# Kernel optimization log

Hardware: AMD Instinct MI355X
Metric: run time of the kernel (lower is better)

## Reference

```python
import jax, jax.numpy as jnp
import numpy as np

B, IN_CH, SLOTS, SLOT_SIZE, READ_SLOTS = 16, 512, 10000, 256, 3


def _fa_params(key, c, scale=0.02):
    k1, k2 = jax.random.split(key)
    return (jax.random.normal(k1, (c, c), jnp.float32) * scale, jnp.zeros((c,), jnp.float32),
            jax.random.normal(k2, (c, c), jnp.float32) * scale, jnp.zeros((c,), jnp.float32))


def fast_attention(x, w1, b1, w2, b2):
    # FastAttention: x * Linear2(softmax(Linear1(x), dim=channel))
    h = jax.nn.softmax(x @ w1 + b1, axis=1)
    return x * (h @ w2 + b2)


def setup_inputs() -> dict:
    key = jax.random.key(0)
    ks = jax.random.split(key, 12)
    s = 0.02
    inp = {}
    inp["inputs"] = jax.random.normal(ks[0], (B, IN_CH), jnp.float32)
    inp["memory"] = jax.random.normal(ks[1], (B, SLOTS, SLOT_SIZE), jnp.float32)
    # read_weights branch: FastAttention(IN_CH) -> Linear(IN_CH, READ_SLOTS*SLOTS) -> tanh
    inp["fa_r_w1"], inp["fa_r_b1"], inp["fa_r_w2"], inp["fa_r_b2"] = _fa_params(ks[2], IN_CH)
    inp["W_read"] = jax.random.normal(ks[3], (IN_CH, READ_SLOTS * SLOTS), jnp.float32) * s
    inp["b_read"] = jnp.zeros((READ_SLOTS * SLOTS,), jnp.float32)
    # update_weights branch: FastAttention(IN_CH) -> Linear(IN_CH, READ_SLOTS) -> sigmoid
    inp["fa_u_w1"], inp["fa_u_b1"], inp["fa_u_w2"], inp["fa_u_b2"] = _fa_params(ks[4], IN_CH)
    inp["W_uw"] = jax.random.normal(ks[5], (IN_CH, READ_SLOTS), jnp.float32) * s
    inp["b_uw"] = jnp.zeros((READ_SLOTS,), jnp.float32)
    # update_memory branch: FastAttention(IN_CH+SLOT_SIZE) -> Linear(., SLOT_SIZE) -> relu
    inp["fa_um_w1"], inp["fa_um_b1"], inp["fa_um_w2"], inp["fa_um_b2"] = _fa_params(ks[6], IN_CH + SLOT_SIZE)
    inp["W_um"] = jax.random.normal(ks[7], (IN_CH + SLOT_SIZE, SLOT_SIZE), jnp.float32) * s
    inp["b_um"] = jnp.zeros((SLOT_SIZE,), jnp.float32)
    # apply_memory branch: FastAttention(2*SLOT_SIZE) -> Linear(., SLOT_SIZE) -> relu
    inp["fa_am_w1"], inp["fa_am_b1"], inp["fa_am_w2"], inp["fa_am_b2"] = _fa_params(ks[8], 2 * SLOT_SIZE)
    inp["W_am"] = jax.random.normal(ks[9], (2 * SLOT_SIZE, SLOT_SIZE), jnp.float32) * s
    inp["b_am"] = jnp.zeros((SLOT_SIZE,), jnp.float32)
    return inp


def reference(inputs, memory,
              fa_r_w1, fa_r_b1, fa_r_w2, fa_r_b2, W_read, b_read,
              fa_u_w1, fa_u_b1, fa_u_w2, fa_u_b2, W_uw, b_uw,
              fa_um_w1, fa_um_b1, fa_um_w2, fa_um_b2, W_um, b_um,
              fa_am_w1, fa_am_b1, fa_am_w2, fa_am_b2, W_am, b_am):
    b = inputs.shape[0]
    # read scores: [B, READ_SLOTS, SLOTS]
    read = jnp.tanh(fast_attention(inputs, fa_r_w1, fa_r_b1, fa_r_w2, fa_r_b2) @ W_read + b_read)
    read = read.reshape(b, READ_SLOTS, SLOTS)
    read_w = jnp.max(read, axis=2)                 # [B, READ_SLOTS]
    read_idx = jnp.argmax(read, axis=2)            # [B, READ_SLOTS] int
    upd_w = jax.nn.sigmoid(fast_attention(inputs, fa_u_w1, fa_u_b1, fa_u_w2, fa_u_b2) @ W_uw + b_uw)
    # gather the selected memory slots: [B, READ_SLOTS, SLOT_SIZE]
    r_all = memory[jnp.arange(b)[:, None], read_idx]
    m = jnp.zeros((b, SLOT_SIZE), inputs.dtype)
    # sequential recurrence over the (small, fixed) read_slots
    for i in range(READ_SLOTS):
        r = r_all[:, i]                            # [B, SLOT_SIZE]
        upd = jax.nn.relu(fast_attention(jnp.concatenate([r, inputs], axis=1),
                                         fa_um_w1, fa_um_b1, fa_um_w2, fa_um_b2) @ W_um + b_um)
        u = upd_w[:, i:i + 1]
        r = u * upd + (1.0 - u) * r
        m = read_w[:, i:i + 1] * jax.nn.relu(fast_attention(jnp.concatenate([r, m], axis=1),
                                                            fa_am_w1, fa_am_b1, fa_am_w2, fa_am_b2) @ W_am + b_am)
    return jnp.tanh(m)
```

## Files before the change

kernel.cpp:

```cpp
#include <hip/hip_runtime.h>
#include <cfloat>
#include <cmath>

constexpr int NTILES = 79;

enum : int {
  WS_XR    = 0,
  WS_UPDW  = 8192,
  WS_READW = 8240,
  WS_PMAX  = 8288,
  WS_PIDX  = 12080,
  WS_RNEW  = 15872,
  WS_M     = 28160,
  WS_XC    = 32256,
  WS_TPA   = 69120,
  WS_HA    = 134656,
  WS_YPA   = 151040,
  WS_TPU   = 216576,
  WS_HU    = 437760,
  WS_YPU   = 474624,
  WS_WPU   = 695808,
  WS_TPM   = 769536,
  WS_HM    = 802304,
  WS_YPM   = 810496,
  WS_WPM   = 843264,
};

__device__ __forceinline__ float wave_sum(float v) {
#pragma unroll
  for (int o = 32; o > 0; o >>= 1) v += __shfl_xor(v, o);
  return v;
}
__device__ __forceinline__ float wave_max(float v) {
#pragma unroll
  for (int o = 32; o > 0; o >>= 1) v = fmaxf(v, __shfl_xor(v, o));
  return v;
}
__device__ __forceinline__ float block_sum(float v, float* red) {
  int lane = threadIdx.x & 63, w = threadIdx.x >> 6, nw = blockDim.x >> 6;
  v = wave_sum(v);
  __syncthreads();
  if (lane == 0) red[w] = v;
  __syncthreads();
  float s = 0.f;
  for (int k = 0; k < nw; k++) s += red[k];
  return s;
}
__device__ __forceinline__ float block_max(float v, float* red) {
  int lane = threadIdx.x & 63, w = threadIdx.x >> 6, nw = blockDim.x >> 6;
  v = wave_max(v);
  __syncthreads();
  if (lane == 0) red[w] = v;
  __syncthreads();
  float s = -FLT_MAX;
  for (int k = 0; k < nw; k++) s = fmaxf(s, red[k]);
  return s;
}

__device__ __forceinline__ void mm_tile16(
    const float* __restrict__ xs,
    const float* __restrict__ W, int ldw,
    int koff, int jbase, float2& ra, float2& rb) {
  int lane = threadIdx.x & 63, w = threadIdx.x >> 6;
  const float* xa = xs + (w * 2) * 128;
  const float* xb = xa + 128;
  const float* Wp = W + (size_t)koff * ldw + jbase + lane * 2;
  float a00 = 0.f, a01 = 0.f, a10 = 0.f, a11 = 0.f;
#pragma unroll 8
  for (int k = 0; k < 128; k++) {
    float2 wv = *(const float2*)(Wp + (size_t)k * ldw);
    float xav = xa[k], xbv = xb[k];
    a00 = fmaf(xav, wv.x, a00); a01 = fmaf(xav, wv.y, a01);
    a10 = fmaf(xbv, wv.x, a10); a11 = fmaf(xbv, wv.y, a11);
  }
  ra = make_float2(a00, a01);
  rb = make_float2(a10, a11);
}
__device__ __forceinline__ void store_tile16(
    float* __restrict__ T, int ldt, int jbase, float2 ra, float2 rb) {
  int lane = threadIdx.x & 63, w = threadIdx.x >> 6;
  int r0 = w * 2, j0 = jbase + lane * 2;
  *(float2*)(T + (size_t)r0 * ldt + j0) = ra;
  *(float2*)(T + (size_t)(r0 + 1) * ldt + j0) = rb;
}

__global__ __launch_bounds__(512) void k_mm1_a(
    const float* __restrict__ x, const float* __restrict__ w1r,
    const float* __restrict__ w1u, float* __restrict__ TPA) {
  __shared__ float xs[16 * 128];
  int jt = blockIdx.x, ks = blockIdx.y, m = blockIdx.z, tid = threadIdx.x;
  for (int t = tid; t < 2048; t += 512) {
    int b = t >> 7, kk = t & 127;
    xs[t] = x[b * 512 + ks * 128 + kk];
  }
  __syncthreads();
  float2 ra, rb;
  mm_tile16(xs, m ? w1u : w1r, 512, ks * 128, jt * 128, ra, rb);
  store_tile16(TPA + (size_t)((m * 4 + ks) * 16) * 512, 512, jt * 128, ra, rb);
}

__global__ __launch_bounds__(512) void k_sm_a(
    const float* __restrict__ TPA, const float* __restrict__ b1r,
    const float* __restrict__ b1u, float* __restrict__ HA) {
  __shared__ float red[16];
  int b = blockIdx.x, m = blockIdx.y, tid = threadIdx.x;
  float t = (m ? b1u : b1r)[tid];
#pragma unroll
  for (int ks = 0; ks < 4; ks++)
    t += TPA[(size_t)((m * 4 + ks) * 16 + b) * 512 + tid];
  float mx = block_max(t, red);
  float e = expf(t - mx);
  float s = block_sum(e, red);
  HA[(size_t)(m * 16 + b) * 512 + tid] = e / s;
}

__global__ __launch_bounds__(512) void k_mm2_a(
    const float* __restrict__ HA, const float* __restrict__ w2r,
    const float* __restrict__ w2u, float* __restrict__ YPA) {
  __shared__ float xs[16 * 128];
  int jt = blockIdx.x, ks = blockIdx.y, m = blockIdx.z, tid = threadIdx.x;
  for (int t = tid; t < 2048; t += 512) {
    int b = t >> 7, kk = t & 127;
    xs[t] = HA[(size_t)(m * 16 + b) * 512 + ks * 128 + kk];
  }
  __syncthreads();
  float2 ra, rb;
  mm_tile16(xs, m ? w2u : w2r, 512, ks * 128, jt * 128, ra, rb);
  store_tile16(YPA + (size_t)((m * 4 + ks) * 16) * 512, 512, jt * 128, ra, rb);
}

__global__ __launch_bounds__(512) void k_fin_a(
    const float* __restrict__ x, const float* __restrict__ YPA,
    const float* __restrict__ b2r, const float* __restrict__ b2u,
    const float* __restrict__ Wuw, const float* __restrict__ buw,
    float* __restrict__ XR, float* __restrict__ UPDW, float* __restrict__ M) {
  __shared__ float red[16];
  int b = blockIdx.x, tid = threadIdx.x;
  float yr = b2r[tid], yu = b2u[tid];
#pragma unroll
  for (int ks = 0; ks < 4; ks++) {
    yr += YPA[(size_t)((0 + ks) * 16 + b) * 512 + tid];
    yu += YPA[(size_t)((4 + ks) * 16 + b) * 512 + tid];
  }
  float xv = x[b * 512 + tid];
  XR[b * 512 + tid] = xv * yr;
  float xu = xv * yu;
  if (tid < 256) M[b * 256 + tid] = 0.f;
  for (int i = 0; i < 3; i++) {
    float si = block_sum(xu * Wuw[tid * 3 + i], red);
    if (tid == 0) UPDW[b * 3 + i] = 1.f / (1.f + expf(-(si + buw[i])));
  }
}

__global__ __launch_bounds__(512) void k_read(
    const float* __restrict__ W, const float* __restrict__ brd,
    const float* __restrict__ xr,
    float* __restrict__ pmax, int* __restrict__ pidx) {
  __shared__ __align__(16) float xs[16 * 512];
  int tid = threadIdx.x, lane = tid & 63, w = tid >> 6;
  int i = blockIdx.y, tile = blockIdx.x;
  {
    const float4* s4 = (const float4*)xr;
    float4* d4 = (float4*)xs;
    for (int t = tid; t < 2048; t += 512) d4[t] = s4[t];
  }
  __syncthreads();
  int b0 = w * 2, b1 = b0 + 1;
  int s0 = tile * 128 + lane * 2;
  int sC = (s0 > 9998) ? 9998 : s0;
  const float* Wp = W + i * 10000 + sC;
  const float* xap = xs + b0 * 512;
  const float* xbp = xs + b1 * 512;
  float a00 = 0.f, a01 = 0.f, a10 = 0.f, a11 = 0.f;
#pragma unroll 8
  for (int c = 0; c < 512; c += 4) {
    float4 xa = *(const float4*)(xap + c);
    float4 xb = *(const float4*)(xbp + c);
    float2 w0 = *(const float2*)(Wp + (size_t)(c + 0) * 30000);
    float2 w1 = *(const float2*)(Wp + (size_t)(c + 1) * 30000);
    float2 w2 = *(const float2*)(Wp + (size_t)(c + 2) * 30000);
    float2 w3 = *(const float2*)(Wp + (size_t)(c + 3) * 30000);
    a00 = fmaf(xa.x, w0.x, a00); a01 = fmaf(xa.x, w0.y, a01);
    a10 = fmaf(xb.x, w0.x, a10); a11 = fmaf(xb.x, w0.y, a11);
    a00 = fmaf(xa.y, w1.x, a00); a01 = fmaf(xa.y, w1.y, a01);
    a10 = fmaf(xb.y, w1.x, a10); a11 = fmaf(xb.y, w1.y, a11);
    a00 = fmaf(xa.z, w2.x, a00); a01 = fmaf(xa.z, w2.y, a01);
    a10 = fmaf(xb.z, w2.x, a10); a11 = fmaf(xb.z, w2.y, a11);
    a00 = fmaf(xa.w, w3.x, a00); a01 = fmaf(xa.w, w3.y, a01);
    a10 = fmaf(xb.w, w3.x, a10); a11 = fmaf(xb.w, w3.y, a11);
  }
  float2 bb = *(const float2*)(brd + i * 10000 + sC);
  bool ok0 = (s0 < 10000), ok1 = (s0 + 1 < 10000);
  float v00 = a00 + bb.x, v01 = a01 + bb.y;
  float v10 = a10 + bb.x, v11 = a11 + bb.y;
  float bv0 = ok0 ? v00 : -FLT_MAX; int bi0 = s0;
  if (ok1 && v01 > bv0) { bv0 = v01; bi0 = s0 + 1; }
  float bv1 = ok0 ? v10 : -FLT_MAX; int bi1 = s0;
  if (ok1 && v11 > bv1) { bv1 = v11; bi1 = s0 + 1; }
#pragma unroll
  for (int o = 32; o > 0; o >>= 1) {
    float ov = __shfl_down(bv0, o); int oi = __shfl_down(bi0, o);
    if (ov > bv0) { bv0 = ov; bi0 = oi; }
    ov = __shfl_down(bv1, o); oi = __shfl_down(bi1, o);
    if (ov > bv1) { bv1 = ov; bi1 = oi; }
  }
  if (lane == 0) {
    int base = (i * 16 + b0) * NTILES + tile;
    pmax[base] = bv0; pidx[base] = bi0;
    base = (i * 16 + b1) * NTILES + tile;
    pmax[base] = bv1; pidx[base] = bi1;
  }
}

__global__ __launch_bounds__(768) void k_gather(
    const float* __restrict__ mem, const float* __restrict__ x,
    const float* __restrict__ pmax, const int* __restrict__ pidx,
    float* __restrict__ READW, float* __restrict__ XC) {
  __shared__ int sidx;
  int bi = blockIdx.x, b = bi / 3, i = bi % 3;
  int tid = threadIdx.x, lane = tid & 63;
  if (tid < 64) {
    float bv = -FLT_MAX; int bix = 0;
    const float* pm = pmax + (i * 16 + b) * NTILES;
    const int* pi = pidx + (i * 16 + b) * NTILES;
    for (int t = lane; t < NTILES; t += 64) {
      float v = pm[t]; int ix = pi[t];
      if (v > bv || (v == bv && ix < bix)) { bv = v; bix = ix; }
    }
#pragma unroll
    for (int o = 32; o > 0; o >>= 1) {
      float ov = __shfl_down(bv, o); int oi = __shfl_down(bix, o);
      if (ov > bv || (ov == bv && oi < bix)) { bv = ov; bix = oi; }
    }
    if (lane == 0) { sidx = bix; READW[bi] = tanhf(bv); }
  }
  __syncthreads();
  if (tid < 256) XC[(size_t)bi * 768 + tid] = mem[((size_t)b * 10000 + sidx) * 256 + tid];
  else           XC[(size_t)bi * 768 + tid] = x[b * 512 + (tid - 256)];
}

__global__ __launch_bounds__(512) void k_mm1_u(
    const float* __restrict__ XC, const float* __restrict__ w1um,
    float* __restrict__ TPU) {
  __shared__ float xs[16 * 128];
  int jt = blockIdx.x, ks = blockIdx.y, g = blockIdx.z, tid = threadIdx.x;
  for (int t = tid; t < 2048; t += 512) {
    int r = t >> 7, kk = t & 127;
    xs[t] = XC[(size_t)(g * 16 + r) * 768 + ks * 128 + kk];
  }
  __syncthreads();
  float2 ra, rb;
  mm_tile16(xs, w1um, 768, ks * 128, jt * 128, ra, rb);
  store_tile16(TPU + (size_t)(ks * 48 + g * 16) * 768, 768, jt * 128, ra, rb);
}

__global__ __launch_bounds__(768) void k_sm_u(
    const float* __restrict__ TPU, const float* __restrict__ b1um,
    float* __restrict__ HU) {
  __shared__ float red[16];
  int bi = blockIdx.x, tid = threadIdx.x;
  float t = b1um[tid];
#pragma unroll
  for (int ks = 0; ks < 6; ks++)
    t += TPU[(size_t)(ks * 48 + bi) * 768 + tid];
  float mx = block_max(t, red);
  float e = expf(t - mx);
  float s = block_sum(e, red);
  HU[(size_t)bi * 768 + tid] = e / s;
}

__global__ __launch_bounds__(512) void k_mm2_u(
    const float* __restrict__ HU, const float* __restrict__ w2um,
    float* __restrict__ YPU) {
  __shared__ float xs[16 * 128];
  int jt = blockIdx.x, ks = blockIdx.y, g = blockIdx.z, tid = threadIdx.x;
  for (int t = tid; t < 2048; t += 512) {
    int r = t >> 7, kk = t & 127;
    xs[t] = HU[(size_t)(g * 16 + r) * 768 + ks * 128 + kk];
  }
  __syncthreads();
  float2 ra, rb;
  mm_tile16(xs, w2um, 768, ks * 128, jt * 128, ra, rb);
  store_tile16(YPU + (size_t)(ks * 48 + g * 16) * 768, 768, jt * 128, ra, rb);
}

__global__ __launch_bounds__(512) void k_wum(
    const float* __restrict__ YPU, const float* __restrict__ XC,
    const float* __restrict__ b2um, const float* __restrict__ Wum,
    float* __restrict__ WPU) {
  __shared__ float xs[16 * 128];
  int jt = blockIdx.x, ks = blockIdx.y, g = blockIdx.z, tid = threadIdx.x;
  for (int t = tid; t < 2048; t += 512) {
    int r = t >> 7, kk = t & 127;
    int bi = g * 16 + r, k = ks * 128 + kk;
    float y = b2um[k];
#pragma unroll
    for (int k2 = 0; k2 < 6; k2++) y += YPU[(size_t)(k2 * 48 + bi) * 768 + k];
    xs[t] = XC[(size_t)bi * 768 + k] * y;
  }
  __syncthreads();
  float2 ra, rb;
  mm_tile16(xs, Wum, 256, ks * 128, jt * 128, ra, rb);
  store_tile16(WPU + (size_t)(ks * 48 + g * 16) * 256, 256, jt * 128, ra, rb);
}

__global__ __launch_bounds__(256) void k_fin_u(
    const float* __restrict__ WPU, const float* __restrict__ XC,
    const float* __restrict__ bum, const float* __restrict__ UPDW,
    float* __restrict__ RNEW) {
  int bi = blockIdx.x, tid = threadIdx.x;
  float s = bum[tid];
#pragma unroll
  for (int ks = 0; ks < 6; ks++)
    s += WPU[(size_t)(ks * 48 + bi) * 256 + tid];
  float u = UPDW[bi];
  RNEW[(size_t)bi * 256 + tid] = u * fmaxf(s, 0.f) + (1.f - u) * XC[(size_t)bi * 768 + tid];
}

__global__ __launch_bounds__(512) void k_mm1_m(
    const float* __restrict__ RNEW, const float* __restrict__ M,
    const float* __restrict__ w1am, float* __restrict__ TPM, int i) {
  __shared__ float xs[16 * 128];
  int jt = blockIdx.x, ks = blockIdx.y, tid = threadIdx.x;
  for (int t = tid; t < 2048; t += 512) {
    int b = t >> 7, kk = t & 127;
    xs[t] = (ks < 2) ? RNEW[(size_t)(b * 3 + i) * 256 + ks * 128 + kk]
                     : M[b * 256 + (ks - 2) * 128 + kk];
  }
  __syncthreads();
  float2 ra, rb;
  mm_tile16(xs, w1am, 512, ks * 128, jt * 128, ra, rb);
  store_tile16(TPM + (size_t)(ks * 16) * 512, 512, jt * 128, ra, rb);
}

__global__ __launch_bounds__(512) void k_sm_m(
    const float* __restrict__ TPM, const float* __restrict__ b1am,
    float* __restrict__ HM) {
  __shared__ float red[16];
  int b = blockIdx.x, tid = threadIdx.x;
  float t = b1am[tid];
#pragma unroll
  for (int ks = 0; ks < 4; ks++)
    t += TPM[(size_t)(ks * 16 + b) * 512 + tid];
  float mx = block_max(t, red);
  float e = expf(t - mx);
  float s = block_sum(e, red);
  HM[(size_t)b * 512 + tid] = e / s;
}

__global__ __launch_bounds__(512) void k_mm2_m(
    const float* __restrict__ HM, const float* __restrict__ w2am,
    float* __restrict__ YPM) {
  __shared__ float xs[16 * 128];
  int jt = blockIdx.x, ks = blockIdx.y, tid = threadIdx.x;
  for (int t = tid; t < 2048; t += 512) {
    int b = t >> 7, kk = t & 127;
    xs[t] = HM[(size_t)b * 512 + ks * 128 + kk];
  }
  __syncthreads();
  float2 ra, rb;
  mm_tile16(xs, w2am, 512, ks * 128, jt * 128, ra, rb);
  store_tile16(YPM + (size_t)(ks * 16) * 512, 512, jt * 128, ra, rb);
}

__global__ __launch_bounds__(512) void k_wam(
    const float* __restrict__ YPM, const float* __restrict__ RNEW,
    const float* __restrict__ M, const float* __restrict__ b2am,
    const float* __restrict__ Wam, float* __restrict__ WPM, int i) {
  __shared__ float xs[16 * 128];
  int jt = blockIdx.x, ks = blockIdx.y, tid = threadIdx.x;
  for (int t = tid; t < 2048; t += 512) {
    int b = t >> 7, kk = t & 127;
    int k = ks * 128 + kk;
    float xc = (ks < 2) ? RNEW[(size_t)(b * 3 + i) * 256 + k]
                        : M[b * 256 + k - 256];
    float y = b2am[k];
#pragma unroll
    for (int k2 = 0; k2 < 4; k2++) y += YPM[(size_t)(k2 * 16 + b) * 512 + k];
    xs[t] = xc * y;
  }
  __syncthreads();
  float2 ra, rb;
  mm_tile16(xs, Wam, 256, ks * 128, jt * 128, ra, rb);
  store_tile16(WPM + (size_t)(ks * 16) * 256, 256, jt * 128, ra, rb);
}

__global__ __launch_bounds__(256) void k_fin_m(
    const float* __restrict__ WPM, const float* __restrict__ bam,
    const float* __restrict__ READW, float* __restrict__ M,
    float* __restrict__ out, int i, int last) {
  int b = blockIdx.x, tid = threadIdx.x;
  float s = bam[tid];
#pragma unroll
  for (int ks = 0; ks < 4; ks++)
    s += WPM[(size_t)(ks * 16 + b) * 256 + tid];
  float mv = READW[b * 3 + i] * fmaxf(s, 0.f);
  M[b * 256 + tid] = mv;
  if (last) out[b * 256 + tid] = tanhf(mv);
}

extern "C" void kernel_launch(void* const* d_in, const int* in_sizes, int n_in,
                              void* d_out, int out_size, void* d_ws, size_t ws_size,
                              hipStream_t stream) {
  const float* x    = (const float*)d_in[0];
  const float* mem  = (const float*)d_in[1];
  const float* w1r  = (const float*)d_in[2];
  const float* b1r  = (const float*)d_in[3];
  const float* w2r  = (const float*)d_in[4];
  const float* b2r  = (const float*)d_in[5];
  const float* Wrd  = (const float*)d_in[6];
  const float* brd  = (const float*)d_in[7];
  const float* w1u  = (const float*)d_in[8];
  const float* b1u  = (const float*)d_in[9];
  const float* w2u  = (const float*)d_in[10];
  const float* b2u  = (const float*)d_in[11];
  const float* Wuw  = (const float*)d_in[12];
  const float* buw  = (const float*)d_in[13];
  const float* w1um = (const float*)d_in[14];
  const float* b1um = (const float*)d_in[15];
  const float* w2um = (const float*)d_in[16];
  const float* b2um = (const float*)d_in[17];
  const float* Wum  = (const float*)d_in[18];
  const float* bum  = (const float*)d_in[19];
  const float* w1am = (const float*)d_in[20];
  const float* b1am = (const float*)d_in[21];
  const float* w2am = (const float*)d_in[22];
  const float* b2am = (const float*)d_in[23];
  const float* Wam  = (const float*)d_in[24];
  const float* bam  = (const float*)d_in[25];

  float* ws   = (float*)d_ws;
  float* XR   = ws + WS_XR;
  float* UPDW = ws + WS_UPDW;
  float* RDW  = ws + WS_READW;
  float* PMAX = ws + WS_PMAX;
  int*   PIDX = (int*)(ws + WS_PIDX);
  float* RNEW = ws + WS_RNEW;
  float* M    = ws + WS_M;
  float* XC   = ws + WS_XC;
  float* TPA  = ws + WS_TPA;
  float* HA   = ws + WS_HA;
  float* YPA  = ws + WS_YPA;
  float* TPU  = ws + WS_TPU;
  float* HU   = ws + WS_HU;
  float* YPU  = ws + WS_YPU;
  float* WPU  = ws + WS_WPU;
  float* TPM  = ws + WS_TPM;
  float* HM   = ws + WS_HM;
  float* YPM  = ws + WS_YPM;
  float* WPM  = ws + WS_WPM;
  float* out  = (float*)d_out;

  k_mm1_a<<<dim3(4, 4, 2), 512, 0, stream>>>(x, w1r, w1u, TPA);
  k_sm_a <<<dim3(16, 2),   512, 0, stream>>>(TPA, b1r, b1u, HA);
  k_mm2_a<<<dim3(4, 4, 2), 512, 0, stream>>>(HA, w2r, w2u, YPA);
  k_fin_a<<<16,            512, 0, stream>>>(x, YPA, b2r, b2u, Wuw, buw,
                                             XR, UPDW, M);
  k_read  <<<dim3(NTILES, 3), 512, 0, stream>>>(Wrd, brd, XR, PMAX, PIDX);
  k_gather<<<48,              768, 0, stream>>>(mem, x, PMAX, PIDX, RDW, XC);
  k_mm1_u<<<dim3(6, 6, 3), 512, 0, stream>>>(XC, w1um, TPU);
  k_sm_u <<<48,            768, 0, stream>>>(TPU, b1um, HU);
  k_mm2_u<<<dim3(6, 6, 3), 512, 0, stream>>>(HU, w2um, YPU);
  k_wum  <<<dim3(2, 6, 3), 512, 0, stream>>>(YPU, XC, b2um, Wum, WPU);
  k_fin_u<<<48,            256, 0, stream>>>(WPU, XC, bum, UPDW, RNEW);
  for (int i = 0; i < 3; i++) {
    k_mm1_m<<<dim3(4, 4), 512, 0, stream>>>(RNEW, M, w1am, TPM, i);
    k_sm_m <<<16,         512, 0, stream>>>(TPM, b1am, HM);
    k_mm2_m<<<dim3(4, 4), 512, 0, stream>>>(HM, w2am, YPM);
    k_wam  <<<dim3(2, 4), 512, 0, stream>>>(YPM, RNEW, M, b2am, Wam, WPM, i);
    k_fin_m<<<16,         256, 0, stream>>>(WPM, bam, RDW, M, out, i, i == 2);
  }
}
```

Before: 508.1 us.

## Fuse each FastAttention branch chain into one per-sample kernel

The split-K matmul, softmax, second matmul and finalize kernels of each branch are replaced by single kernels (kA, kC, kD). In these, one block per sample (or per sample and slot) computes both FastAttention matvecs, the softmax and the output linear layer, keeping intermediates in shared memory. This removes about twenty launches and the global-memory round trips for partial sums, and drops the separate M zeroing step (i==0 handles it). The cost is far less parallelism: only 16 to 48 blocks, each streaming full weight matrices with a serial k loop, so each step may become latency or bandwidth bound per CU.

Result: slower. 1.199 ms (+135.9%).

```diff
diff --git a/kernel.cpp b/kernel.cpp
--- a/kernel.cpp
+++ b/kernel.cpp
@@ -12,18 +12,6 @@
   WS_PIDX  = 12080,
   WS_RNEW  = 15872,
   WS_M     = 28160,
-  WS_XC    = 32256,
-  WS_TPA   = 69120,
-  WS_HA    = 134656,
-  WS_YPA   = 151040,
-  WS_TPU   = 216576,
-  WS_HU    = 437760,
-  WS_YPU   = 474624,
-  WS_WPU   = 695808,
-  WS_TPM   = 769536,
-  WS_HM    = 802304,
-  WS_YPM   = 810496,
-  WS_WPM   = 843264,
 };
 
 __device__ __forceinline__ float wave_sum(float v) {
@@ -57,98 +45,48 @@
   return s;
 }
 
-__device__ __forceinline__ void mm_tile16(
-    const float* __restrict__ xs,
-    const float* __restrict__ W, int ldw,
-    int koff, int jbase, float2& ra, float2& rb) {
-  int lane = threadIdx.x & 63, w = threadIdx.x >> 6;
-  const float* xa = xs + (w * 2) * 128;
-  const float* xb = xa + 128;
-  const float* Wp = W + (size_t)koff * ldw + jbase + lane * 2;
-  float a00 = 0.f, a01 = 0.f, a10 = 0.f, a11 = 0.f;
-#pragma unroll 8
-  for (int k = 0; k < 128; k++) {
-    float2 wv = *(const float2*)(Wp + (size_t)k * ldw);
-    float xav = xa[k], xbv = xb[k];
-    a00 = fmaf(xav, wv.x, a00); a01 = fmaf(xav, wv.y, a01);
-    a10 = fmaf(xbv, wv.x, a10); a11 = fmaf(xbv, wv.y, a11);
-  }
-  ra = make_float2(a00, a01);
-  rb = make_float2(a10, a11);
-}
-__device__ __forceinline__ void store_tile16(
-    float* __restrict__ T, int ldt, int jbase, float2 ra, float2 rb) {
-  int lane = threadIdx.x & 63, w = threadIdx.x >> 6;
-  int r0 = w * 2, j0 = jbase + lane * 2;
-  *(float2*)(T + (size_t)r0 * ldt + j0) = ra;
-  *(float2*)(T + (size_t)(r0 + 1) * ldt + j0) = rb;
-}
-
-__global__ __launch_bounds__(512) void k_mm1_a(
-    const float* __restrict__ x, const float* __restrict__ w1r,
-    const float* __restrict__ w1u, float* __restrict__ TPA) {
-  __shared__ float xs[16 * 128];
-  int jt = blockIdx.x, ks = blockIdx.y, m = blockIdx.z, tid = threadIdx.x;
-  for (int t = tid; t < 2048; t += 512) {
-    int b = t >> 7, kk = t & 127;
-    xs[t] = x[b * 512 + ks * 128 + kk];
-  }
-  __syncthreads();
-  float2 ra, rb;
-  mm_tile16(xs, m ? w1u : w1r, 512, ks * 128, jt * 128, ra, rb);
-  store_tile16(TPA + (size_t)((m * 4 + ks) * 16) * 512, 512, jt * 128, ra, rb);
-}
-
-__global__ __launch_bounds__(512) void k_sm_a(
-    const float* __restrict__ TPA, const float* __restrict__ b1r,
-    const float* __restrict__ b1u, float* __restrict__ HA) {
-  __shared__ float red[16];
-  int b = blockIdx.x, m = blockIdx.y, tid = threadIdx.x;
-  float t = (m ? b1u : b1r)[tid];
-#pragma unroll
-  for (int ks = 0; ks < 4; ks++)
-    t += TPA[(size_t)((m * 4 + ks) * 16 + b) * 512 + tid];
-  float mx = block_max(t, red);
-  float e = expf(t - mx);
+__global__ __launch_bounds__(512) void kA(
+    const float* __restrict__ x,
+    const float* __restrict__ w1r, const float* __restrict__ b1r,
+    const float* __restrict__ w2r, const float* __restrict__ b2r,
+    const float* __restrict__ w1u, const float* __restrict__ b1u,
+    const float* __restrict__ w2u, const float* __restrict__ b2u,
+    const float* __restrict__ Wuw, const float* __restrict__ buw,
+    float* __restrict__ XR, float* __restrict__ UPDW) {
+  __shared__ float xl[512], hl[512], red[16];
+  int bid = blockIdx.x, m = bid >> 4, b = bid & 15, tid = threadIdx.x;
+  const float* w1 = m ? w1u : w1r;  const float* b1 = m ? b1u : b1r;
+  const float* w2 = m ? w2u : w2r;  const float* b2 = m ? b2u : b2r;
+  float xv = x[b * 512 + tid];
+  xl[tid] = xv;
+  __syncthreads();
+  float a0 = 0.f, a1 = 0.f;
+#pragma unroll 8
+  for (int k = 0; k < 256; k++)   a0 = fmaf(xl[k], w1[(size_t)k * 512 + tid], a0);
+#pragma unroll 8
+  for (int k = 256; k < 512; k++) a1 = fmaf(xl[k], w1[(size_t)k * 512 + tid], a1);
+  float v = a0 + a1 + b1[tid];
+  float mx = block_max(v, red);
+  float e = expf(v - mx);
   float s = block_sum(e, red);
-  HA[(size_t)(m * 16 + b) * 512 + tid] = e / s;
-}
-
-__global__ __launch_bounds__(512) void k_mm2_a(
-    const float* __restrict__ HA, const float* __restrict__ w2r,
-    const float* __restrict__ w2u, float* __restrict__ YPA) {
-  __shared__ float xs[16 * 128];
-  int jt = blockIdx.x, ks = blockIdx.y, m = blockIdx.z, tid = threadIdx.x;
-  for (int t = tid; t < 2048; t += 512) {
-    int b = t >> 7, kk = t & 127;
-    xs[t] = HA[(size_t)(m * 16 + b) * 512 + ks * 128 + kk];
-  }
-  __syncthreads();
-  float2 ra, rb;
-  mm_tile16(xs, m ? w2u : w2r, 512, ks * 128, jt * 128, ra, rb);
-  store_tile16(YPA + (size_t)((m * 4 + ks) * 16) * 512, 512, jt * 128, ra, rb);
-}
-
-__global__ __launch_bounds__(512) void k_fin_a(
-    const float* __restrict__ x, const float* __restrict__ YPA,
-    const float* __restrict__ b2r, const float* __restrict__ b2u,
-    const float* __restrict__ Wuw, const float* __restrict__ buw,
-    float* __restrict__ XR, float* __restrict__ UPDW, float* __restrict__ M) {
-  __shared__ float red[16];
-  int b = blockIdx.x, tid = threadIdx.x;
-  float yr = b2r[tid], yu = b2u[tid];
-#pragma unroll
-  for (int ks = 0; ks < 4; ks++) {
-    yr += YPA[(size_t)((0 + ks) * 16 + b) * 512 + tid];
-    yu += YPA[(size_t)((4 + ks) * 16 + b) * 512 + tid];
-  }
-  float xv = x[b * 512 + tid];
-  XR[b * 512 + tid] = xv * yr;
-  float xu = xv * yu;
-  if (tid < 256) M[b * 256 + tid] = 0.f;
-  for (int i = 0; i < 3; i++) {
-    float si = block_sum(xu * Wuw[tid * 3 + i], red);
-    if (tid == 0) UPDW[b * 3 + i] = 1.f / (1.f + expf(-(si + buw[i])));
+  hl[tid] = e / s;
+  __syncthreads();
+  float y0 = 0.f, y1 = 0.f;
+#pragma unroll 8
+  for (int k = 0; k < 256; k++)   y0 = fmaf(hl[k], w2[(size_t)k * 512 + tid], y0);
+#pragma unroll 8
+  for (int k = 256; k < 512; k++) y1 = fmaf(hl[k], w2[(size_t)k * 512 + tid], y1);
+  float o = xv * (y0 + y1 + b2[tid]);
+  if (m == 0) {
+    XR[b * 512 + tid] = o;
+  } else {
+    __syncthreads();
+    hl[tid] = o;
+    __syncthreads();
+    for (int i = 0; i < 3; i++) {
+      float si = block_sum(hl[tid] * Wuw[tid * 3 + i], red);
+      if (tid == 0) UPDW[b * 3 + i] = 1.f / (1.f + expf(-(si + buw[i])));
+    }
   }
 }
 
@@ -212,12 +150,17 @@
   }
 }
 
-__global__ __launch_bounds__(768) void k_gather(
+__global__ __launch_bounds__(512) void kC(
     const float* __restrict__ mem, const float* __restrict__ x,
     const float* __restrict__ pmax, const int* __restrict__ pidx,
-    float* __restrict__ READW, float* __restrict__ XC) {
+    const float* __restrict__ w1um, const float* __restrict__ b1um,
+    const float* __restrict__ w2um, const float* __restrict__ b2um,
+    const float* __restrict__ Wum, const float* __restrict__ bum,
+    const float* __restrict__ UPDW,
+    float* __restrict__ RDW, float* __restrict__ RNEW) {
+  __shared__ float xcl[768], hl[768], xul[768], part[512], red[16];
   __shared__ int sidx;
-  int bi = blockIdx.x, b = bi / 3, i = bi % 3;
+  int bid = blockIdx.x, b = bid / 3, i = bid % 3;
   int tid = threadIdx.x, lane = tid & 63;
   if (tid < 64) {
     float bv = -FLT_MAX; int bix = 0;
@@ -232,171 +175,113 @@
       float ov = __shfl_down(bv, o); int oi = __shfl_down(bix, o);
       if (ov > bv || (ov == bv && oi < bix)) { bv = ov; bix = oi; }
     }
-    if (lane == 0) { sidx = bix; READW[bi] = tanhf(bv); }
-  }
-  __syncthreads();
-  if (tid < 256) XC[(size_t)bi * 768 + tid] = mem[((size_t)b * 10000 + sidx) * 256 + tid];
-  else           XC[(size_t)bi * 768 + tid] = x[b * 512 + (tid - 256)];
-}
-
-__global__ __launch_bounds__(512) void k_mm1_u(
-    const float* __restrict__ XC, const float* __restrict__ w1um,
-    float* __restrict__ TPU) {
-  __shared__ float xs[16 * 128];
-  int jt = blockIdx.x, ks = blockIdx.y, g = blockIdx.z, tid = threadIdx.x;
-  for (int t = tid; t < 2048; t += 512) {
-    int r = t >> 7, kk = t & 127;
-    xs[t] = XC[(size_t)(g * 16 + r) * 768 + ks * 128 + kk];
-  }
-  __syncthreads();
-  float2 ra, rb;
-  mm_tile16(xs, w1um, 768, ks * 128, jt * 128, ra, rb);
-  store_tile16(TPU + (size_t)(ks * 48 + g * 16) * 768, 768, jt * 128, ra, rb);
-}
-
-__global__ __launch_bounds__(768) void k_sm_u(
-    const float* __restrict__ TPU, const float* __restrict__ b1um,
-    float* __restrict__ HU) {
-  __shared__ float red[16];
-  int bi = blockIdx.x, tid = threadIdx.x;
-  float t = b1um[tid];
-#pragma unroll
-  for (int ks = 0; ks < 6; ks++)
-    t += TPU[(size_t)(ks * 48 + bi) * 768 + tid];
-  float mx = block_max(t, red);
-  float e = expf(t - mx);
+    if (lane == 0) { sidx = bix; RDW[bid] = tanhf(bv); }
+  }
+  __syncthreads();
+  xcl[tid] = (tid < 256) ? mem[((size_t)b * 10000 + sidx) * 256 + tid]
+                         : x[b * 512 + tid - 256];
+  if (tid < 256) xcl[512 + tid] = x[b * 512 + 256 + tid];
+  __syncthreads();
+  float a0 = 0.f, a0b = 0.f, a1 = 0.f, a1b = 0.f;
+#pragma unroll 8
+  for (int k = 0; k < 384; k++) {
+    float xk = xcl[k]; const float* Wr = w1um + (size_t)k * 768;
+    a0 = fmaf(xk, Wr[tid], a0);
+    if (tid < 256) a1 = fmaf(xk, Wr[512 + tid], a1);
+  }
+#pragma unroll 8
+  for (int k = 384; k < 768; k++) {
+    float xk = xcl[k]; const float* Wr = w1um + (size_t)k * 768;
+    a0b = fmaf(xk, Wr[tid], a0b);
+    if (tid < 256) a1b = fmaf(xk, Wr[512 + tid], a1b);
+  }
+  float v0 = a0 + a0b + b1um[tid];
+  float v1 = (tid < 256) ? (a1 + a1b + b1um[512 + tid]) : -FLT_MAX;
+  float mx = block_max(fmaxf(v0, v1), red);
+  float e0 = expf(v0 - mx);
+  float e1 = (tid < 256) ? expf(v1 - mx) : 0.f;
+  float s = block_sum(e0 + e1, red);
+  float inv = 1.f / s;
+  hl[tid] = e0 * inv;
+  if (tid < 256) hl[512 + tid] = e1 * inv;
+  __syncthreads();
+  float y0 = 0.f, y0b = 0.f, y1 = 0.f, y1b = 0.f;
+#pragma unroll 8
+  for (int k = 0; k < 384; k++) {
+    float hk = hl[k]; const float* Wr = w2um + (size_t)k * 768;
+    y0 = fmaf(hk, Wr[tid], y0);
+    if (tid < 256) y1 = fmaf(hk, Wr[512 + tid], y1);
+  }
+#pragma unroll 8
+  for (int k = 384; k < 768; k++) {
+    float hk = hl[k]; const float* Wr = w2um + (size_t)k * 768;
+    y0b = fmaf(hk, Wr[tid], y0b);
+    if (tid < 256) y1b = fmaf(hk, Wr[512 + tid], y1b);
+  }
+  xul[tid] = xcl[tid] * (y0 + y0b + b2um[tid]);
+  if (tid < 256) xul[512 + tid] = xcl[512 + tid] * (y1 + y1b + b2um[512 + tid]);
+  __syncthreads();
+  int j = tid & 255, kh = tid >> 8;
+  float acc = 0.f;
+#pragma unroll 8
+  for (int k = kh * 384; k < kh * 384 + 384; k++)
+    acc = fmaf(xul[k], Wum[(size_t)k * 256 + j], acc);
+  part[tid] = acc;
+  __syncthreads();
+  if (tid < 256) {
+    float sf = part[tid] + part[tid + 256] + bum[tid];
+    float u = UPDW[b * 3 + i];
+    RNEW[(size_t)(b * 3 + i) * 256 + tid] =
+        u * fmaxf(sf, 0.f) + (1.f - u) * xcl[tid];
+  }
+}
+
+__global__ __launch_bounds__(512) void kD(
+    const float* __restrict__ RNEW, const float* __restrict__ Mbuf,
+    const float* __restrict__ w1am, const float* __restrict__ b1am,
+    const float* __restrict__ w2am, const float* __restrict__ b2am,
+    const float* __restrict__ Wam, const float* __restrict__ bam,
+    const float* __restrict__ RDW, float* __restrict__ Mout,
+    float* __restrict__ out, int i, int last) {
+  __shared__ float xcl[512], hl[512], part[512], red[16];
+  int b = blockIdx.x, tid = threadIdx.x;
+  float xv = (tid < 256) ? RNEW[(size_t)(b * 3 + i) * 256 + tid]
+                         : (i == 0 ? 0.f : Mbuf[b * 256 + tid - 256]);
+  xcl[tid] = xv;
+  __syncthreads();
+  float a0 = 0.f, a1 = 0.f;
+#pragma unroll 8
+  for (int k = 0; k < 256; k++)   a0 = fmaf(xcl[k], w1am[(size_t)k * 512 + tid], a0);
+#pragma unroll 8
+  for (int k = 256; k < 512; k++) a1 = fmaf(xcl[k], w1am[(size_t)k * 512 + tid], a1);
+  float v = a0 + a1 + b1am[tid];
+  float mx = block_max(v, red);
+  float e = expf(v - mx);
   float s = block_sum(e, red);
-  HU[(size_t)bi * 768 + tid] = e / s;
-}
-
-__global__ __launch_bounds__(512) void k_mm2_u(
-    const float* __restrict__ HU, const float* __restrict__ w2um,
-    float* __restrict__ YPU) {
-  __shared__ float xs[16 * 128];
-  int jt = blockIdx.x, ks = blockIdx.y, g = blockIdx.z, tid = threadIdx.x;
-  for (int t = tid; t < 2048; t += 512) {
-    int r = t >> 7, kk = t & 127;
-    xs[t] = HU[(size_t)(g * 16 + r) * 768 + ks * 128 + kk];
-  }
-  __syncthreads();
-  float2 ra, rb;
-  mm_tile16(xs, w2um, 768, ks * 128, jt * 128, ra, rb);
-  store_tile16(YPU + (size_t)(ks * 48 + g * 16) * 768, 768, jt * 128, ra, rb);
-}
-
-__global__ __launch_bounds__(512) void k_wum(
-    const float* __restrict__ YPU, const float* __restrict__ XC,
-    const float* __restrict__ b2um, const float* __restrict__ Wum,
-    float* __restrict__ WPU) {
-  __shared__ float xs[16 * 128];
-  int jt = blockIdx.x, ks = blockIdx.y, g = blockIdx.z, tid = threadIdx.x;
-  for (int t = tid; t < 2048; t += 512) {
-    int r = t >> 7, kk = t & 127;
-    int bi = g * 16 + r, k = ks * 128 + kk;
-    float y = b2um[k];
-#pragma unroll
-    for (int k2 = 0; k2 < 6; k2++) y += YPU[(size_t)(k2 * 48 + bi) * 768 + k];
-    xs[t] = XC[(size_t)bi * 768 + k] * y;
-  }
-  __syncthreads();
-  float2 ra, rb;
-  mm_tile16(xs, Wum, 256, ks * 128, jt * 128, ra, rb);
-  store_tile16(WPU + (size_t)(ks * 48 + g * 16) * 256, 256, jt * 128, ra, rb);
-}
-
-__global__ __launch_bounds__(256) void k_fin_u(
-    const float* __restrict__ WPU, const float* __restrict__ XC,
-    const float* __restrict__ bum, const float* __restrict__ UPDW,
-    float* __restrict__ RNEW) {
-  int bi = blockIdx.x, tid = threadIdx.x;
-  float s = bum[tid];
-#pragma unroll
-  for (int ks = 0; ks < 6; ks++)
-    s += WPU[(size_t)(ks * 48 + bi) * 256 + tid];
-  float u = UPDW[bi];
-  RNEW[(size_t)bi * 256 + tid] = u * fmaxf(s, 0.f) + (1.f - u) * XC[(size_t)bi * 768 + tid];
-}
-
-__global__ __launch_bounds__(512) void k_mm1_m(
-    const float* __restrict__ RNEW, const float* __restrict__ M,
-    const float* __restrict__ w1am, float* __restrict__ TPM, int i) {
-  __shared__ float xs[16 * 128];
-  int jt = blockIdx.x, ks = blockIdx.y, tid = threadIdx.x;
-  for (int t = tid; t < 2048; t += 512) {
-    int b = t >> 7, kk = t & 127;
-    xs[t] = (ks < 2) ? RNEW[(size_t)(b * 3 + i) * 256 + ks * 128 + kk]
-                     : M[b * 256 + (ks - 2) * 128 + kk];
-  }
-  __syncthreads();
-  float2 ra, rb;
-  mm_tile16(xs, w1am, 512, ks * 128, jt * 128, ra, rb);
-  store_tile16(TPM + (size_t)(ks * 16) * 512, 512, jt * 128, ra, rb);
-}
-
-__global__ __launch_bounds__(512) void k_sm_m(
-    const float* __restrict__ TPM, const float* __restrict__ b1am,
-    float* __restrict__ HM) {
-  __shared__ float red[16];
-  int b = blockIdx.x, tid = threadIdx.x;
-  float t = b1am[tid];
-#pragma unroll
-  for (int ks = 0; ks < 4; ks++)
-    t += TPM[(size_t)(ks * 16 + b) * 512 + tid];
-  float mx = block_max(t, red);
-  float e = expf(t - mx);
-  float s = block_sum(e, red);
-  HM[(size_t)b * 512 + tid] = e / s;
-}
-
-__global__ __launch_bounds__(512) void k_mm2_m(
-    const float* __restrict__ HM, const float* __restrict__ w2am,
-    float* __restrict__ YPM) {
-  __shared__ float xs[16 * 128];
-  int jt = blockIdx.x, ks = blockIdx.y, tid = threadIdx.x;
-  for (int t = tid; t < 2048; t += 512) {
-    int b = t >> 7, kk = t & 127;
-    xs[t] = HM[(size_t)b * 512 + ks * 128 + kk];
-  }
-  __syncthreads();
-  float2 ra, rb;
-  mm_tile16(xs, w2am, 512, ks * 128, jt * 128, ra, rb);
-  store_tile16(YPM + (size_t)(ks * 16) * 512, 512, jt * 128, ra, rb);
-}
-
-__global__ __launch_bounds__(512) void k_wam(
-    const float* __restrict__ YPM, const float* __restrict__ RNEW,
-    const float* __restrict__ M, const float* __restrict__ b2am,
-    const float* __restrict__ Wam, float* __restrict__ WPM, int i) {
-  __shared__ float xs[16 * 128];
-  int jt = blockIdx.x, ks = blockIdx.y, tid = threadIdx.x;
-  for (int t = tid; t < 2048; t += 512) {
-    int b = t >> 7, kk = t & 127;
-    int k = ks * 128 + kk;
-    float xc = (ks < 2) ? RNEW[(size_t)(b * 3 + i) * 256 + k]
-                        : M[b * 256 + k - 256];
-    float y = b2am[k];
-#pragma unroll
-    for (int k2 = 0; k2 < 4; k2++) y += YPM[(size_t)(k2 * 16 + b) * 512 + k];
-    xs[t] = xc * y;
-  }
-  __syncthreads();
-  float2 ra, rb;
-  mm_tile16(xs, Wam, 256, ks * 128, jt * 128, ra, rb);
-  store_tile16(WPM + (size_t)(ks * 16) * 256, 256, jt * 128, ra, rb);
-}
-
-__global__ __launch_bounds__(256) void k_fin_m(
-    const float* __restrict__ WPM, const float* __restrict__ bam,
-    const float* __restrict__ READW, float* __restrict__ M,
-    float* __restrict__ out, int i, int last) {
-  int b = blockIdx.x, tid = threadIdx.x;
-  float s = bam[tid];
-#pragma unroll
-  for (int ks = 0; ks < 4; ks++)
-    s += WPM[(size_t)(ks * 16 + b) * 256 + tid];
-  float mv = READW[b * 3 + i] * fmaxf(s, 0.f);
-  M[b * 256 + tid] = mv;
-  if (last) out[b * 256 + tid] = tanhf(mv);
+  hl[tid] = e / s;
+  __syncthreads();
+  float y0 = 0.f, y1 = 0.f;
+#pragma unroll 8
+  for (int k = 0; k < 256; k++)   y0 = fmaf(hl[k], w2am[(size_t)k * 512 + tid], y0);
+#pragma unroll 8
+  for (int k = 256; k < 512; k++) y1 = fmaf(hl[k], w2am[(size_t)k * 512 + tid], y1);
+  float xa = xv * (y0 + y1 + b2am[tid]);
+  __syncthreads();
+  hl[tid] = xa;
+  __syncthreads();
+  int j = tid & 255, kh = tid >> 8;
+  float acc = 0.f;
+#pragma unroll 8
+  for (int k = kh * 256; k < kh * 256 + 256; k++)
+    acc = fmaf(hl[k], Wam[(size_t)k * 256 + j], acc);
+  part[tid] = acc;
+  __syncthreads();
+  if (tid < 256) {
+    float sf = part[tid] + part[tid + 256] + bam[tid];
+    float mv = RDW[b * 3 + i] * fmaxf(sf, 0.f);
+    Mout[b * 256 + tid] = mv;
+    if (last) out[b * 256 + tid] = tanhf(mv);
+  }
 }
 
 extern "C" void kernel_launch(void* const* d_in, const int* in_sizes, int n_in,
@@ -437,37 +322,16 @@
   int*   PIDX = (int*)(ws + WS_PIDX);
   float* RNEW = ws + WS_RNEW;
   float* M    = ws + WS_M;
-  float* XC   = ws + WS_XC;
-  float* TPA  = ws + WS_TPA;
-  float* HA   = ws + WS_HA;
-  float* YPA  = ws + WS_YPA;
-  float* TPU  = ws + WS_TPU;
-  float* HU   = ws + WS_HU;
-  float* YPU  = ws + WS_YPU;
-  float* WPU  = ws + WS_WPU;
-  float* TPM  = ws + WS_TPM;
-  float* HM   = ws + WS_HM;
-  float* YPM  = ws + WS_YPM;
-  float* WPM  = ws + WS_WPM;
   float* out  = (float*)d_out;
 
-  k_mm1_a<<<dim3(4, 4, 2), 512, 0, stream>>>(x, w1r, w1u, TPA);
-  k_sm_a <<<dim3(16, 2),   512, 0, stream>>>(TPA, b1r, b1u, HA);
-  k_mm2_a<<<dim3(4, 4, 2), 512, 0, stream>>>(HA, w2r, w2u, YPA);
-  k_fin_a<<<16,            512, 0, stream>>>(x, YPA, b2r, b2u, Wuw, buw,
-                                             XR, UPDW, M);
-  k_read  <<<dim3(NTILES, 3), 512, 0, stream>>>(Wrd, brd, XR, PMAX, PIDX);
-  k_gather<<<48,              768, 0, stream>>>(mem, x, PMAX, PIDX, RDW, XC);
-  k_mm1_u<<<dim3(6, 6, 3), 512, 0, stream>>>(XC, w1um, TPU);
-  k_sm_u <<<48,            768, 0, stream>>>(TPU, b1um, HU);
-  k_mm2_u<<<dim3(6, 6, 3), 512, 0, stream>>>(HU, w2um, YPU);
-  k_wum  <<<dim3(2, 6, 3), 512, 0, stream>>>(YPU, XC, b2um, Wum, WPU);
-  k_fin_u<<<48,            256, 0, stream>>>(WPU, XC, bum, UPDW, RNEW);
-  for (int i = 0; i < 3; i++) {
-    k_mm1_m<<<dim3(4, 4), 512, 0, stream>>>(RNEW, M, w1am, TPM, i);
-    k_sm_m <<<16,         512, 0, stream>>>(TPM, b1am, HM);
-    k_mm2_m<<<dim3(4, 4), 512, 0, stream>>>(HM, w2am, YPM);
-    k_wam  <<<dim3(2, 4), 512, 0, stream>>>(YPM, RNEW, M, b2am, Wam, WPM, i);
-    k_fin_m<<<16,         256, 0, stream>>>(WPM, bam, RDW, M, out, i, i == 2);
-  }
-}
+  kA    <<<32,                512, 0, stream>>>(x, w1r, b1r, w2r, b2r,
+                                                w1u, b1u, w2u, b2u, Wuw, buw,
+                                                XR, UPDW);
+  k_read<<<dim3(NTILES, 3),   512, 0, stream>>>(Wrd, brd, XR, PMAX, PIDX);
+  kC    <<<48,                512, 0, stream>>>(mem, x, PMAX, PIDX,
+                                                w1um, b1um, w2um, b2um, Wum, bum,
+                                                UPDW, RDW, RNEW);
+  for (int i = 0; i < 3; i++)
+    kD  <<<16,                512, 0, stream>>>(RNEW, M, w1am, b1am, w2am, b2am,
+                                                Wam, bam, RDW, M, out, i, i == 2);
+}
```
